# Kernel optimization log

Hardware: AMD Instinct MI355X
Metric: run time of the kernel (lower is better)

Reference implementation:

```python
import jax, jax.numpy as jnp
import numpy as np

N_NODES = 100000
N_EDGES = 1600000
N_GRAPHS = 256
IN_DIM = 64
HID = 128
LIN_HID = 128
OUT_H1, OUT_H2 = 128, 258
RELU_COEF = 0.05


def _lin_init(key, fan_in, fan_out, bias=True):
    k1, k2 = jax.random.split(key)
    bound = 1.0 / np.sqrt(fan_in)
    W = jax.random.uniform(k1, (fan_in, fan_out), minval=-bound, maxval=bound, dtype=jnp.float32)
    if bias:
        b = jax.random.uniform(k2, (fan_out,), minval=-bound, maxval=bound, dtype=jnp.float32)
        return W, b
    return W


def setup_inputs() -> dict:
    key = jax.random.key(0)
    ks = jax.random.split(key, 12)
    x = jax.random.normal(ks[0], (N_NODES, IN_DIM), dtype=jnp.float32)
    edge_index = jax.random.randint(ks[1], (2, N_EDGES), 0, N_NODES)
    batch = jnp.sort(jax.random.randint(ks[2], (N_NODES,), 0, N_GRAPHS))
    edge_attr = jax.random.uniform(ks[3], (N_EDGES,), dtype=jnp.float32)
    # GraphConv params: lin_rel (bias) applied to aggregated messages, lin_root (no bias)
    Wrel1, brel1 = _lin_init(ks[4], IN_DIM, HID)
    Wroot1 = _lin_init(ks[5], IN_DIM, HID, bias=False)
    Wrel2, brel2 = _lin_init(ks[6], HID, HID)
    Wroot2 = _lin_init(ks[7], HID, HID, bias=False)
    Wsig, bsig = _lin_init(ks[8], HID + IN_DIM, LIN_HID)
    Wtanh, btanh = _lin_init(ks[9], HID + IN_DIM, LIN_HID)
    Wf1, bf1 = _lin_init(ks[10], LIN_HID, OUT_H1)
    k11, k12 = jax.random.split(ks[11])
    Wf2, bf2 = _lin_init(k11, OUT_H1, OUT_H2)
    Wout, bout = _lin_init(k12, OUT_H2, 1)
    return dict(x=x, edge_index=edge_index, batch=batch, edge_attr=edge_attr,
                Wrel1=Wrel1, brel1=brel1, Wroot1=Wroot1,
                Wrel2=Wrel2, brel2=brel2, Wroot2=Wroot2,
                Wsig=Wsig, bsig=bsig, Wtanh=Wtanh, btanh=btanh,
                Wf1=Wf1, bf1=bf1, Wf2=Wf2, bf2=bf2, Wout=Wout, bout=bout)


def _leaky(v):
    return jnp.where(v > 0, v, RELU_COEF * v)


def _graph_conv(x, src, dst, w, Wrel, brel, Wroot):
    # out_i = Wrel @ sum_{j->i} w_ji * x_j + brel + Wroot @ x_i  (PyG GraphConv, aggr='add')
    msg = x[src] * w[:, None]                                   # [E, d]
    agg = jax.ops.segment_sum(msg, dst, num_segments=N_NODES)   # [N, d]
    return agg @ Wrel + brel + x @ Wroot


def reference(x, edge_index, batch, edge_attr,
              Wrel1, brel1, Wroot1, Wrel2, brel2, Wroot2,
              Wsig, bsig, Wtanh, btanh, Wf1, bf1, Wf2, bf2, Wout, bout):
    src, dst = edge_index[0], edge_index[1]
    x0 = x
    h = _leaky(_graph_conv(x0, src, dst, edge_attr, Wrel1, brel1, Wroot1))
    h = _leaky(_graph_conv(h, src, dst, edge_attr, Wrel2, brel2, Wroot2))
    h = jnp.concatenate([h, x0], axis=1)                        # [N, HID+IN_DIM]
    sx = jnp.clip(h @ Wsig + bsig, -30.0, 30.0)
    g = jax.nn.sigmoid(-sx) * jnp.tanh(h @ Wtanh + btanh)       # 1/(1+exp(sx)) == sigmoid(-sx)
    pooled = jax.ops.segment_sum(g, batch, num_segments=N_GRAPHS)  # [G, LIN_HID]
    f = _leaky(pooled @ Wf1 + bf1)
    f = _leaky(f @ Wf2 + bf2)
    out = jax.nn.sigmoid(f @ Wout + bout)                       # [G, 1]
    return out
```

## Files before the change

kernel.cpp:

```cpp
#include <hip/hip_runtime.h>
#include <cstdint>

#define RELU_COEF 0.05f
#define LEAKY(v) ((v) > 0.f ? (v) : RELU_COEF * (v))

typedef __attribute__((ext_vector_type(8))) short short8;
typedef __attribute__((ext_vector_type(4))) float f32x4;

#define MFMA(acc, a, b) \
    acc = __builtin_amdgcn_mfma_f32_16x16x32_bf16(a, b, acc, 0, 0, 0)

__device__ inline ushort f2bf(float f) {
    union { float f; uint32_t u; } v; v.f = f;
    return (ushort)((v.u + 0x7FFFu + ((v.u >> 16) & 1u)) >> 16);
}
__device__ inline float bf2f(ushort h) {
    union { uint32_t u; float f; } v; v.u = ((uint32_t)h) << 16;
    return v.f;
}
__device__ inline void split8(const float* p, short8& h8, short8& l8) {
    float4 a = *(const float4*)p;
    float4 b = *(const float4*)(p + 4);
    float v[8] = {a.x, a.y, a.z, a.w, b.x, b.y, b.z, b.w};
    short8 hh, ll;
#pragma unroll
    for (int i = 0; i < 8; ++i) {
        ushort hi = f2bf(v[i]);
        hh[i] = (short)hi;
        ll[i] = (short)f2bf(v[i] - bf2f(hi));
    }
    h8 = hh; l8 = ll;
}

__global__ __launch_bounds__(256) void hist_kernel(
    const int* __restrict__ ei, int* __restrict__ deg, int E)
{
    int e = blockIdx.x * 256 + threadIdx.x;
    if (e >= E) return;
    atomicAdd(&deg[ei[(size_t)E + e]], 1);
}

__global__ __launch_bounds__(256) void scan1_kernel(
    const int* __restrict__ in, int* __restrict__ out, int* __restrict__ bsum, int N)
{
    __shared__ int ts[256];
    int tid = threadIdx.x;
    int base = blockIdx.x * 1024 + tid * 4;
    int v[4];
    int s = 0;
#pragma unroll
    for (int j = 0; j < 4; ++j) {
        int idx = base + j;
        v[j] = (idx < N) ? in[idx] : 0;
        s += v[j];
    }
    ts[tid] = s;
    __syncthreads();
    for (int off = 1; off < 256; off <<= 1) {
        int t = (tid >= off) ? ts[tid - off] : 0;
        __syncthreads();
        ts[tid] += t;
        __syncthreads();
    }
    int excl = ts[tid] - s;
    if (tid == 255) bsum[blockIdx.x] = ts[255];
    int run = excl;
#pragma unroll
    for (int j = 0; j < 4; ++j) {
        int idx = base + j;
        if (idx < N) out[idx] = run;
        run += v[j];
    }
}

__global__ __launch_bounds__(512) void scan2_kernel(int* bsum, int nb)
{
    __shared__ int ts[512];
    int tid = threadIdx.x;
    int v = (tid < nb) ? bsum[tid] : 0;
    ts[tid] = v;
    __syncthreads();
    for (int off = 1; off < 512; off <<= 1) {
        int t = (tid >= off) ? ts[tid - off] : 0;
        __syncthreads();
        ts[tid] += t;
        __syncthreads();
    }
    if (tid < nb) bsum[tid] = ts[tid] - v;
}

__global__ __launch_bounds__(256) void scan3_kernel(
    int* __restrict__ rowptr, const int* __restrict__ bsum, int N, int E)
{
    int idx = blockIdx.x * 256 + threadIdx.x;
    if (idx < N) rowptr[idx] += bsum[idx >> 10];
    if (idx == 0) rowptr[N] = E;
}

#define CHUNK 4096
__global__ __launch_bounds__(256) void partA_kernel(
    const int* __restrict__ ei, const float* __restrict__ ea,
    const int* __restrict__ rowptr, int* __restrict__ bucketCursor,
    int2* __restrict__ csw2, int E, int NB)
{
    __shared__ int cnt[256];
    __shared__ int scanx[256];
    __shared__ int runc[256];
    __shared__ int gbase[256];
    __shared__ int2 staged[CHUNK];
    __shared__ unsigned char bkt[CHUNK];

    int tid = threadIdx.x;
    long long base = (long long)blockIdx.x * CHUNK;
    int cntHere = (int)((E - base) < CHUNK ? (E - base) : CHUNK);

    cnt[tid] = 0; runc[tid] = 0;
    __syncthreads();

    for (int i = tid; i < cntHere; i += 256) {
        int d = ei[(size_t)E + base + i];
        atomicAdd(&cnt[d >> 9], 1);
    }
    __syncthreads();

    int v = cnt[tid];
    scanx[tid] = v;
    __syncthreads();
    for (int off = 1; off < 256; off <<= 1) {
        int t = (tid >= off) ? scanx[tid - off] : 0;
        __syncthreads();
        scanx[tid] += t;
        __syncthreads();
    }
    int excl = scanx[tid] - v;
    if (tid < NB && v > 0)
        gbase[tid] = rowptr[tid << 9] + atomicAdd(&bucketCursor[tid], v);
    scanx[tid] = excl;
    __syncthreads();

    for (int i = tid; i < cntHere; i += 256) {
        long long e = base + i;
        int d = ei[(size_t)E + e];
        int b = d >> 9;
        int idx = scanx[b] + atomicAdd(&runc[b], 1);
        staged[idx] = make_int2(((d & 511) << 17) | ei[e], __float_as_int(ea[e]));
        bkt[idx] = (unsigned char)b;
    }
    __syncthreads();

    for (int i = tid; i < cntHere; i += 256) {
        int b = bkt[i];
        csw2[gbase[b] + (i - scanx[b])] = staged[i];
    }
}

__global__ __launch_bounds__(256) void partB_kernel(
    const int2* __restrict__ csw2, const int* __restrict__ rowptr,
    int2* __restrict__ csw, int N, int E)
{
    __shared__ int cur[512];
    int b = blockIdx.x;
    int tid = threadIdx.x;
    int node0 = b << 9;
    int nNodes = N - node0; if (nNodes > 512) nNodes = 512;
    for (int i = tid; i < nNodes; i += 256)
        cur[i] = rowptr[node0 + i];
    __syncthreads();
    int start = rowptr[node0];
    int end = (node0 + 512 >= N) ? E : rowptr[node0 + 512];
    for (int i = start + tid; i < end; i += 256) {
        int2 p = csw2[i];
        int dstLow = (int)(((unsigned)p.x) >> 17);
        int src = p.x & 0x1FFFF;
        int pos = atomicAdd(&cur[dstLow], 1);
        csw[pos] = make_int2(src, p.y);
    }
}

__global__ __launch_bounds__(256) void xbf_kernel(
    const float* __restrict__ x, ushort* __restrict__ xbf, int total4)
{
    int i = blockIdx.x * 256 + threadIdx.x;
    if (i >= total4) return;
    float4 v = *(const float4*)(x + (size_t)i * 4);
    ushort4 h;
    h.x = f2bf(v.x); h.y = f2bf(v.y); h.z = f2bf(v.z); h.w = f2bf(v.w);
    *(ushort4*)(xbf + (size_t)i * 4) = h;
}

__global__ __launch_bounds__(256) void prep_weights_kernel(
    const float* __restrict__ Wrel1, const float* __restrict__ Wroot1,
    const float* __restrict__ Wrel2, const float* __restrict__ Wroot2,
    const float* __restrict__ Wsig, const float* __restrict__ Wtanh,
    ushort* __restrict__ W1f, ushort* __restrict__ W2f, ushort* __restrict__ Wgf)
{
    int gid = blockIdx.x * 256 + threadIdx.x;
    if (gid < 32768) {
        int e = gid & 7, nn = (gid >> 3) & 127, kc = (gid >> 10) & 3;
        int hl = (gid >> 12) & 1, kk = gid >> 13;
        int k = kk * 32 + kc * 8 + e;
        float v = (k < 64) ? Wrel1[(size_t)k * 128 + nn]
                           : Wroot1[(size_t)(k - 64) * 128 + nn];
        ushort hi = f2bf(v);
        W1f[gid] = hl ? f2bf(v - bf2f(hi)) : hi;
        return;
    }
    int g2 = gid - 32768;
    if (g2 < 65536) {
        int e = g2 & 7, nn = (g2 >> 3) & 127, kc = (g2 >> 10) & 3;
        int hl = (g2 >> 12) & 1, kk = g2 >> 13;
        int k = kk * 32 + kc * 8 + e;
        float v = (k < 128) ? Wrel2[(size_t)k * 128 + nn]
                            : Wroot2[(size_t)(k - 128) * 128 + nn];
        ushort hi = f2bf(v);
        W2f[g2] = hl ? f2bf(v - bf2f(hi)) : hi;
        return;
    }
    int g3 = g2 - 65536;
    if (g3 < 98304) {
        int e = g3 & 7, nn = (g3 >> 3) & 127, kc = (g3 >> 10) & 3;
        int p = (g3 >> 12) & 3, kk = g3 >> 14;
        int k = kk * 32 + kc * 8 + e;
        float v = (p < 2) ? Wsig[(size_t)k * 128 + nn]
                          : Wtanh[(size_t)k * 128 + nn];
        ushort hi = f2bf(v);
        Wgf[g3] = (p & 1) ? f2bf(v - bf2f(hi)) : hi;
    }
}

__global__ __launch_bounds__(256) void conv1_fused_kernel(
    const float* __restrict__ x, const ushort* __restrict__ xbf,
    const int* __restrict__ rowptr, const int2* __restrict__ csw,
    const ushort* __restrict__ W1f, const float* __restrict__ brel,
    ushort* __restrict__ h1bf, int n)
{
    __shared__ __align__(16) float agg[32 * 68];

    int tid = threadIdx.x;
    int lane = tid & 63;
    int wv = tid >> 6;
    int mr = lane & 15;
    int kc = lane >> 4;
    int i0 = blockIdx.x * 32;

    {
        int q = tid & 15;
        int g = tid >> 4;
#pragma unroll
        for (int it = 0; it < 2; ++it) {
            int rl = it * 16 + g;
            int node = i0 + rl;
            float ax = 0.f, ay = 0.f, az = 0.f, aw = 0.f;
            if (node < n) {
                int b = rowptr[node], e = rowptr[node + 1];
                for (int cb = b; cb < e; cb += 16) {
                    int cnt = e - cb; if (cnt > 16) cnt = 16;
                    int sIdx = 0; float sW = 0.f;
                    if (q < cnt) {
                        int2 p = csw[cb + q];
                        sIdx = p.x; sW = __int_as_float(p.y);
                    }
                    int j = 0;
                    for (; j + 8 <= cnt; j += 8) {
                        int si[8]; float wi[8]; ushort4 fv[8];
#pragma unroll
                        for (int u = 0; u < 8; ++u) {
                            si[u] = __shfl(sIdx, j + u, 16);
                            wi[u] = __shfl(sW, j + u, 16);
                        }
#pragma unroll
                        for (int u = 0; u < 8; ++u)
                            fv[u] = *(const ushort4*)(xbf + (size_t)si[u] * 64 + q * 4);
#pragma unroll
                        for (int u = 0; u < 8; ++u) {
                            ax += wi[u] * bf2f(fv[u].x);
                            ay += wi[u] * bf2f(fv[u].y);
                            az += wi[u] * bf2f(fv[u].z);
                            aw += wi[u] * bf2f(fv[u].w);
                        }
                    }
                    for (; j < cnt; ++j) {
                        int s0 = __shfl(sIdx, j, 16); float w0 = __shfl(sW, j, 16);
                        ushort4 f0 = *(const ushort4*)(xbf + (size_t)s0 * 64 + q * 4);
                        ax += w0 * bf2f(f0.x); ay += w0 * bf2f(f0.y);
                        az += w0 * bf2f(f0.z); aw += w0 * bf2f(f0.w);
                    }
                }
            }
            *(float4*)&agg[rl * 68 + q * 4] = make_float4(ax, ay, az, aw);
        }
    }
    __syncthreads();

    int t0 = wv * 2;
    const ushort* Wp = W1f + kc * 1024 + t0 * 128 + mr * 8;
    f32x4 acc[2][2] = {};

#pragma unroll
    for (int kk = 0; kk < 2; ++kk) {
        short8 bH0 = *(const short8*)(Wp + kk * 8192);
        short8 bH1 = *(const short8*)(Wp + kk * 8192 + 128);
        short8 bL0 = *(const short8*)(Wp + kk * 8192 + 4096);
        short8 bL1 = *(const short8*)(Wp + kk * 8192 + 4096 + 128);
#pragma unroll
        for (int sub = 0; sub < 2; ++sub) {
            short8 aH, aL;
            split8(&agg[(sub * 16 + mr) * 68 + kk * 32 + kc * 8], aH, aL);
            MFMA(acc[sub][0], aH, bH0); MFMA(acc[sub][0], aH, bL0); MFMA(acc[sub][0], aL, bH0);
            MFMA(acc[sub][1], aH, bH1); MFMA(acc[sub][1], aH, bL1); MFMA(acc[sub][1], aL, bH1);
        }
    }
#pragma unroll
    for (int kk = 2; kk < 4; ++kk) {
        short8 bH0 = *(const short8*)(Wp + kk * 8192);
        short8 bH1 = *(const short8*)(Wp + kk * 8192 + 128);
        short8 bL0 = *(const short8*)(Wp + kk * 8192 + 4096);
        short8 bL1 = *(const short8*)(Wp + kk * 8192 + 4096 + 128);
#pragma unroll
        for (int sub = 0; sub < 2; ++sub) {
            int row = i0 + sub * 16 + mr; if (row > n - 1) row = n - 1;
            short8 aH, aL;
            split8(x + (size_t)row * 64 + (kk - 2) * 32 + kc * 8, aH, aL);
            MFMA(acc[sub][0], aH, bH0); MFMA(acc[sub][0], aH, bL0); MFMA(acc[sub][0], aL, bH0);
            MFMA(acc[sub][1], aH, bH1); MFMA(acc[sub][1], aH, bL1); MFMA(acc[sub][1], aL, bH1);
        }
    }

#pragma unroll
    for (int tt = 0; tt < 2; ++tt) {
        int c = (t0 + tt) * 16 + mr;
        float bv = brel[c];
#pragma unroll
        for (int sub = 0; sub < 2; ++sub)
#pragma unroll
            for (int j = 0; j < 4; ++j) {
                int r = i0 + sub * 16 + kc * 4 + j;
                if (r < n)
                    h1bf[(size_t)r * 128 + c] = f2bf(LEAKY(acc[sub][tt][j] + bv));
            }
    }
}

__global__ __launch_bounds__(256) void conv2_gate_kernel(
    const ushort* __restrict__ h1bf, const float* __restrict__ x,
    const int* __restrict__ rowptr, const int2* __restrict__ csw,
    const ushort* __restrict__ W2f, const float* __restrict__ brel,
    const ushort* __restrict__ Wgf, const float* __restrict__ bsig,
    const float* __restrict__ btanh, const int* __restrict__ batch,
    float* __restrict__ pooled, int n)
{
    __shared__ __align__(16) float agg[32 * 132];
    __shared__ int bS[32];
    float* gs = agg;

    int tid = threadIdx.x;
    int lane = tid & 63;
    int wv = tid >> 6;
    int mr = lane & 15;
    int kc = lane >> 4;
    int i0 = blockIdx.x * 32;

    {
        int q = tid & 31;
        int g = tid >> 5;
#pragma unroll
        for (int it = 0; it < 4; ++it) {
            int rl = it * 8 + g;
            int node = i0 + rl;
            float ax = 0.f, ay = 0.f, az = 0.f, aw = 0.f;
            if (node < n) {
                int b = rowptr[node], e = rowptr[node + 1];
                for (int cb = b; cb < e; cb += 32) {
                    int cnt = e - cb; if (cnt > 32) cnt = 32;
                    int sIdx = 0; float sW = 0.f;
                    if (q < cnt) {
                        int2 p = csw[cb + q];
                        sIdx = p.x; sW = __int_as_float(p.y);
                    }
                    int j = 0;
                    for (; j + 8 <= cnt; j += 8) {
                        int si[8]; float wi[8]; ushort4 fv[8];
#pragma unroll
                        for (int u = 0; u < 8; ++u) {
                            si[u] = __shfl(sIdx, j + u, 32);
                            wi[u] = __shfl(sW, j + u, 32);
                        }
#pragma unroll
                        for (int u = 0; u < 8; ++u)
                            fv[u] = *(const ushort4*)(h1bf + (size_t)si[u] * 128 + q * 4);
#pragma unroll
                        for (int u = 0; u < 8; ++u) {
                            ax += wi[u] * bf2f(fv[u].x);
                            ay += wi[u] * bf2f(fv[u].y);
                            az += wi[u] * bf2f(fv[u].z);
                            aw += wi[u] * bf2f(fv[u].w);
                        }
                    }
                    for (; j < cnt; ++j) {
                        int s0 = __shfl(sIdx, j, 32); float w0 = __shfl(sW, j, 32);
                        ushort4 f0 = *(const ushort4*)(h1bf + (size_t)s0 * 128 + q * 4);
                        ax += w0 * bf2f(f0.x); ay += w0 * bf2f(f0.y);
                        az += w0 * bf2f(f0.z); aw += w0 * bf2f(f0.w);
                    }
                }
            }
            *(float4*)&agg[rl * 132 + q * 4] = make_float4(ax, ay, az, aw);
        }
    }
    if (tid < 32) {
        int r = i0 + tid;
        bS[tid] = (r < n) ? batch[r] : -1;
    }
    __syncthreads();

    int t0 = wv * 2;

    f32x4 acc[2][2] = {};
    {
        const ushort* Wp = W2f + kc * 1024 + t0 * 128 + mr * 8;
#pragma unroll
        for (int kk = 0; kk < 4; ++kk) {
            short8 bH0 = *(const short8*)(Wp + kk * 8192);
            short8 bH1 = *(const short8*)(Wp + kk * 8192 + 128);
            short8 bL0 = *(const short8*)(Wp + kk * 8192 + 4096);
            short8 bL1 = *(const short8*)(Wp + kk * 8192 + 4096 + 128);
#pragma unroll
            for (int sub = 0; sub < 2; ++sub) {
                short8 aH, aL;
                split8(&agg[(sub * 16 + mr) * 132 + kk * 32 + kc * 8], aH, aL);
                MFMA(acc[sub][0], aH, bH0); MFMA(acc[sub][0], aH, bL0); MFMA(acc[sub][0], aL, bH0);
                MFMA(acc[sub][1], aH, bH1); MFMA(acc[sub][1], aH, bL1); MFMA(acc[sub][1], aL, bH1);
            }
        }
#pragma unroll
        for (int kk = 4; kk < 8; ++kk) {
            short8 bH0 = *(const short8*)(Wp + kk * 8192);
            short8 bH1 = *(const short8*)(Wp + kk * 8192 + 128);
            short8 bL0 = *(const short8*)(Wp + kk * 8192 + 4096);
            short8 bL1 = *(const short8*)(Wp + kk * 8192 + 4096 + 128);
#pragma unroll
            for (int sub = 0; sub < 2; ++sub) {
                int row = i0 + sub * 16 + mr; if (row > n - 1) row = n - 1;
                short8 aH = *(const short8*)(h1bf + (size_t)row * 128 + (kk - 4) * 32 + kc * 8);
                MFMA(acc[sub][0], aH, bH0); MFMA(acc[sub][0], aH, bL0);
                MFMA(acc[sub][1], aH, bH1); MFMA(acc[sub][1], aH, bL1);
            }
        }
    }
    __syncthreads();

#pragma unroll
    for (int tt = 0; tt < 2; ++tt) {
        int c = (t0 + tt) * 16 + mr;
        float bv = brel[c];
#pragma unroll
        for (int sub = 0; sub < 2; ++sub)
#pragma unroll
            for (int j = 0; j < 4; ++j) {
                int rl = sub * 16 + kc * 4 + j;
                agg[rl * 132 + c] = LEAKY(acc[sub][tt][j] + bv);
            }
    }
    __syncthreads();

    f32x4 as[2][2] = {}, at_[2][2] = {};
    {
        const ushort* Wp = Wgf + kc * 1024 + t0 * 128 + mr * 8;
#pragma unroll
        for (int kk = 0; kk < 4; ++kk) {
            short8 sH0 = *(const short8*)(Wp + kk * 16384);
            short8 sH1 = *(const short8*)(Wp + kk * 16384 + 128);
            short8 sL0 = *(const short8*)(Wp + kk * 16384 + 4096);
            short8 sL1 = *(const short8*)(Wp + kk * 16384 + 4096 + 128);
            short8 tH0 = *(const short8*)(Wp + kk * 16384 + 8192);
            short8 tH1 = *(const short8*)(Wp + kk * 16384 + 8192 + 128);
            short8 tL0 = *(const short8*)(Wp + kk * 16384 + 12288);
            short8 tL1 = *(const short8*)(Wp + kk * 16384 + 12288 + 128);
#pragma unroll
            for (int sub = 0; sub < 2; ++sub) {
                short8 aH, aL;
                split8(&agg[(sub * 16 + mr) * 132 + kk * 32 + kc * 8], aH, aL);
                MFMA(as[sub][0], aH, sH0); MFMA(as[sub][0], aH, sL0); MFMA(as[sub][0], aL, sH0);
                MFMA(as[sub][1], aH, sH1); MFMA(as[sub][1], aH, sL1); MFMA(as[sub][1], aL, sH1);
                MFMA(at_[sub][0], aH, tH0); MFMA(at_[sub][0], aH, tL0); MFMA(at_[sub][0], aL, tH0);
                MFMA(at_[sub][1], aH, tH1); MFMA(at_[sub][1], aH, tL1); MFMA(at_[sub][1], aL, tH1);
            }
        }
#pragma unroll
        for (int kk = 4; kk < 6; ++kk) {
            short8 sH0 = *(const short8*)(Wp + kk * 16384);
            short8 sH1 = *(const short8*)(Wp + kk * 16384 + 128);
            short8 sL0 = *(const short8*)(Wp + kk * 16384 + 4096);
            short8 sL1 = *(const short8*)(Wp + kk * 16384 + 4096 + 128);
            short8 tH0 = *(const short8*)(Wp + kk * 16384 + 8192);
            short8 tH1 = *(const short8*)(Wp + kk * 16384 + 8192 + 128);
            short8 tL0 = *(const short8*)(Wp + kk * 16384 + 12288);
            short8 tL1 = *(const short8*)(Wp + kk * 16384 + 12288 + 128);
#pragma unroll
            for (int sub = 0; sub < 2; ++sub) {
                int row = i0 + sub * 16 + mr; if (row > n - 1) row = n - 1;
                short8 aH, aL;
                split8(x + (size_t)row * 64 + (kk - 4) * 32 + kc * 8, aH, aL);
                MFMA(as[sub][0], aH, sH0); MFMA(as[sub][0], aH, sL0); MFMA(as[sub][0], aL, sH0);
                MFMA(as[sub][1], aH, sH1); MFMA(as[sub][1], aH, sL1); MFMA(as[sub][1], aL, sH1);
                MFMA(at_[sub][0], aH, tH0); MFMA(at_[sub][0], aH, tL0); MFMA(at_[sub][0], aL, tH0);
                MFMA(at_[sub][1], aH, tH1); MFMA(at_[sub][1], aH, tL1); MFMA(at_[sub][1], aL, tH1);
            }
        }
    }
    __syncthreads();

#pragma unroll
    for (int tt = 0; tt < 2; ++tt) {
        int c = (t0 + tt) * 16 + mr;
        float bsv = bsig[c], btv = btanh[c];
#pragma unroll
        for (int sub = 0; sub < 2; ++sub)
#pragma unroll
            for (int j = 0; j < 4; ++j) {
                int rl = sub * 16 + kc * 4 + j;
                float s = as[sub][tt][j] + bsv;
                s = fminf(fmaxf(s, -30.f), 30.f);
                float ta = at_[sub][tt][j] + btv;
                ta = fminf(fmaxf(ta, -15.f), 15.f);
                float e2 = __expf(2.f * ta);
                float th = (e2 - 1.f) / (e2 + 1.f);
                gs[rl * 128 + c] = th / (1.f + __expf(s));
            }
    }
    __syncthreads();

    int j = tid & 127;
    int m0 = (tid >> 7) * 16;
    float acc2 = 0.f;
    int cur = -1;
    for (int m = m0; m < m0 + 16; ++m) {
        int b = bS[m];
        if (b < 0) break;
        if (b != cur) {
            if (cur >= 0) atomicAdd(&pooled[(size_t)cur * 128 + j], acc2);
            cur = b;
            acc2 = 0.f;
        }
        acc2 += gs[m * 128 + j];
    }
    if (cur >= 0) atomicAdd(&pooled[(size_t)cur * 128 + j], acc2);
}

__global__ __launch_bounds__(256) void mlp_kernel(
    const float* __restrict__ pooled,
    const float* __restrict__ Wf1, const float* __restrict__ bf1,
    const float* __restrict__ Wf2, const float* __restrict__ bf2,
    const float* __restrict__ Wout, const float* __restrict__ bout,
    float* __restrict__ out)
{
    __shared__ float p[128];
    __shared__ float f1[128];
    __shared__ float f2[258];
    __shared__ float red[4];

    int g = blockIdx.x;
    int tid = threadIdx.x;

    if (tid < 128) p[tid] = pooled[(size_t)g * 128 + tid];
    __syncthreads();

    if (tid < 128) {
        float a = bf1[tid];
        for (int k = 0; k < 128; ++k) a += p[k] * Wf1[k * 128 + tid];
        f1[tid] = LEAKY(a);
    }
    __syncthreads();

    for (int j = tid; j < 258; j += 256) {
        float a = bf2[j];
        for (int k = 0; k < 128; ++k) a += f1[k] * Wf2[k * 258 + j];
        f2[j] = LEAKY(a);
    }
    __syncthreads();

    float a = 0.f;
    for (int j = tid; j < 258; j += 256) a += f2[j] * Wout[j];
#pragma unroll
    for (int off = 32; off > 0; off >>= 1) a += __shfl_down(a, off, 64);
    if ((tid & 63) == 0) red[tid >> 6] = a;
    __syncthreads();
    if (tid == 0) {
        float v = red[0] + red[1] + red[2] + red[3] + bout[0];
        out[g] = 1.f / (1.f + expf(-v));
    }
}

extern "C" void kernel_launch(void* const* d_in, const int* in_sizes, int n_in,
                              void* d_out, int out_size, void* d_ws, size_t ws_size,
                              hipStream_t stream)
{
    const float* x     = (const float*)d_in[0];
    const int*   ei    = (const int*)d_in[1];
    const int*   batch = (const int*)d_in[2];
    const float* ea    = (const float*)d_in[3];
    const float* Wrel1 = (const float*)d_in[4];
    const float* brel1 = (const float*)d_in[5];
    const float* Wroot1= (const float*)d_in[6];
    const float* Wrel2 = (const float*)d_in[7];
    const float* brel2 = (const float*)d_in[8];
    const float* Wroot2= (const float*)d_in[9];
    const float* Wsig  = (const float*)d_in[10];
    const float* bsig  = (const float*)d_in[11];
    const float* Wtanh = (const float*)d_in[12];
    const float* btanh = (const float*)d_in[13];
    const float* Wf1   = (const float*)d_in[14];
    const float* bf1   = (const float*)d_in[15];
    const float* Wf2   = (const float*)d_in[16];
    const float* bf2   = (const float*)d_in[17];
    const float* Wout  = (const float*)d_in[18];
    const float* bout  = (const float*)d_in[19];

    int N = in_sizes[2];
    int E = in_sizes[3];
    int NB = (N + 511) / 512;

    char* base = (char*)d_ws;
    size_t off = 0;
    auto alloc = [&](size_t bytes) {
        char* p = base + off;
        off += (bytes + 255) & ~(size_t)255;
        return p;
    };
    ushort*   h1bf  = (ushort*)alloc((size_t)N * 128 * 2);
    ushort*   xbf   = (ushort*)alloc((size_t)N * 64 * 2);
    int*      rowptr= (int*)alloc((size_t)(N + 1) * 4);
    int*      cursor= (int*)alloc((size_t)N * 4);
    int*      bsum  = (int*)alloc(512 * 4);
    int*      bcur  = (int*)alloc(256 * 4);
    int2*     csw   = (int2*)alloc((size_t)E * 8);
    int2*     csw2  = (int2*)alloc((size_t)E * 8);
    ushort*   W1f   = (ushort*)alloc(32768 * 2);
    ushort*   W2f   = (ushort*)alloc(65536 * 2);
    ushort*   Wgf   = (ushort*)alloc(98304 * 2);
    float*    pooled= (float*)alloc(256 * 128 * 4);

    int eblk = (E + 255) / 256;
    int nblk1 = (N + 1023) / 1024;
    int cblk = (N + 31) / 32;
    int ablk = (E + CHUNK - 1) / CHUNK;

    hipMemsetAsync(cursor, 0, (size_t)N * sizeof(int), stream);
    hipMemsetAsync(bcur, 0, 256 * sizeof(int), stream);
    hipMemsetAsync(pooled, 0, (size_t)256 * 128 * sizeof(float), stream);

    prep_weights_kernel<<<768, 256, 0, stream>>>(Wrel1, Wroot1, Wrel2, Wroot2,
                                                 Wsig, Wtanh, W1f, W2f, Wgf);
    xbf_kernel<<<(N * 16 + 255) / 256, 256, 0, stream>>>(x, xbf, N * 16);

    hist_kernel<<<eblk, 256, 0, stream>>>(ei, cursor, E);
    scan1_kernel<<<nblk1, 256, 0, stream>>>(cursor, rowptr, bsum, N);
    scan2_kernel<<<1, 512, 0, stream>>>(bsum, nblk1);
    scan3_kernel<<<(N + 255) / 256, 256, 0, stream>>>(rowptr, bsum, N, E);
    partA_kernel<<<ablk, 256, 0, stream>>>(ei, ea, rowptr, bcur, csw2, E, NB);
    partB_kernel<<<NB, 256, 0, stream>>>(csw2, rowptr, csw, N, E);

    conv1_fused_kernel<<<cblk, 256, 0, stream>>>(x, xbf, rowptr, csw,
                                                 W1f, brel1, h1bf, N);

    conv2_gate_kernel<<<cblk, 256, 0, stream>>>(h1bf, x, rowptr, csw,
                                                W2f, brel2, Wgf, bsig, btanh,
                                                batch, pooled, N);

    mlp_kernel<<<256, 256, 0, stream>>>(pooled, Wf1, bf1, Wf2, bf2, Wout, bout,
                                        (float*)d_out);
}
```

Measured before the change: 355.9 us.

## Build CSR via bucket histogram and per-bucket local scan; prefetch edge chunks

Replaces the per-node global atomic degree histogram and three-kernel scan with a shared-memory per-bucket histogram, a single 256-entry scan, and a per-bucket local histogram and scan inside partB that also writes rowptr. This removes 1.6M global atomics, an N-sized memset, and several launches. Separately, the conv gather loops now prefetch the next chunk of CSR edge entries while processing the current one, to hide load latency. The cost is an extra pass over csw2 in partB.

```diff
diff --git a/kernel.cpp b/kernel.cpp
--- a/kernel.cpp
+++ b/kernel.cpp
@@ -32,29 +32,30 @@
     h8 = hh; l8 = ll;
 }
 
-__global__ __launch_bounds__(256) void hist_kernel(
-    const int* __restrict__ ei, int* __restrict__ deg, int E)
-{
-    int e = blockIdx.x * 256 + threadIdx.x;
-    if (e >= E) return;
-    atomicAdd(&deg[ei[(size_t)E + e]], 1);
-}
-
-__global__ __launch_bounds__(256) void scan1_kernel(
-    const int* __restrict__ in, int* __restrict__ out, int* __restrict__ bsum, int N)
+#define CHUNK 4096
+
+__global__ __launch_bounds__(256) void bhist_kernel(
+    const int* __restrict__ ei, int* __restrict__ bhist, int E)
+{
+    __shared__ int cnt[256];
+    int tid = threadIdx.x;
+    cnt[tid] = 0;
+    __syncthreads();
+    long long base = (long long)blockIdx.x * CHUNK;
+    int cntHere = (int)((E - base) < CHUNK ? (E - base) : CHUNK);
+    for (int i = tid; i < cntHere; i += 256)
+        atomicAdd(&cnt[ei[(size_t)E + base + i] >> 9], 1);
+    __syncthreads();
+    if (cnt[tid] > 0) atomicAdd(&bhist[tid], cnt[tid]);
+}
+
+__global__ __launch_bounds__(256) void bscan_kernel(
+    const int* __restrict__ bhist, int* __restrict__ bptr, int E)
 {
     __shared__ int ts[256];
     int tid = threadIdx.x;
-    int base = blockIdx.x * 1024 + tid * 4;
-    int v[4];
-    int s = 0;
-#pragma unroll
-    for (int j = 0; j < 4; ++j) {
-        int idx = base + j;
-        v[j] = (idx < N) ? in[idx] : 0;
-        s += v[j];
-    }
-    ts[tid] = s;
+    int v = bhist[tid];
+    ts[tid] = v;
     __syncthreads();
     for (int off = 1; off < 256; off <<= 1) {
         int t = (tid >= off) ? ts[tid - off] : 0;
@@ -62,45 +63,13 @@
         ts[tid] += t;
         __syncthreads();
     }
-    int excl = ts[tid] - s;
-    if (tid == 255) bsum[blockIdx.x] = ts[255];
-    int run = excl;
-#pragma unroll
-    for (int j = 0; j < 4; ++j) {
-        int idx = base + j;
-        if (idx < N) out[idx] = run;
-        run += v[j];
-    }
-}
-
-__global__ __launch_bounds__(512) void scan2_kernel(int* bsum, int nb)
-{
-    __shared__ int ts[512];
-    int tid = threadIdx.x;
-    int v = (tid < nb) ? bsum[tid] : 0;
-    ts[tid] = v;
-    __syncthreads();
-    for (int off = 1; off < 512; off <<= 1) {
-        int t = (tid >= off) ? ts[tid - off] : 0;
-        __syncthreads();
-        ts[tid] += t;
-        __syncthreads();
-    }
-    if (tid < nb) bsum[tid] = ts[tid] - v;
-}
-
-__global__ __launch_bounds__(256) void scan3_kernel(
-    int* __restrict__ rowptr, const int* __restrict__ bsum, int N, int E)
-{
-    int idx = blockIdx.x * 256 + threadIdx.x;
-    if (idx < N) rowptr[idx] += bsum[idx >> 10];
-    if (idx == 0) rowptr[N] = E;
-}
-
-#define CHUNK 4096
+    bptr[tid] = ts[tid] - v;
+    if (tid == 255) bptr[256] = E;
+}
+
 __global__ __launch_bounds__(256) void partA_kernel(
     const int* __restrict__ ei, const float* __restrict__ ea,
-    const int* __restrict__ rowptr, int* __restrict__ bucketCursor,
+    const int* __restrict__ bptr, int* __restrict__ bucketCursor,
     int2* __restrict__ csw2, int E, int NB)
 {
     __shared__ int cnt[256];
@@ -134,7 +103,7 @@
     }
     int excl = scanx[tid] - v;
     if (tid < NB && v > 0)
-        gbase[tid] = rowptr[tid << 9] + atomicAdd(&bucketCursor[tid], v);
+        gbase[tid] = bptr[tid] + atomicAdd(&bucketCursor[tid], v);
     scanx[tid] = excl;
     __syncthreads();
 
@@ -155,19 +124,47 @@
 }
 
 __global__ __launch_bounds__(256) void partB_kernel(
-    const int2* __restrict__ csw2, const int* __restrict__ rowptr,
-    int2* __restrict__ csw, int N, int E)
-{
+    const int2* __restrict__ csw2, const int* __restrict__ bptr,
+    int* __restrict__ rowptr, int2* __restrict__ csw, int N, int E)
+{
+    __shared__ int hist[512];
     __shared__ int cur[512];
+    __shared__ int ts[256];
+
     int b = blockIdx.x;
     int tid = threadIdx.x;
     int node0 = b << 9;
+    int start = bptr[b], end = bptr[b + 1];
+
+    hist[tid] = 0; hist[tid + 256] = 0;
+    __syncthreads();
+    for (int i = start + tid; i < end; i += 256) {
+        int2 p = csw2[i];
+        atomicAdd(&hist[((unsigned)p.x) >> 17], 1);
+    }
+    __syncthreads();
+
+    int v0 = hist[2 * tid], v1 = hist[2 * tid + 1];
+    int s = v0 + v1;
+    ts[tid] = s;
+    __syncthreads();
+    for (int off = 1; off < 256; off <<= 1) {
+        int t = (tid >= off) ? ts[tid - off] : 0;
+        __syncthreads();
+        ts[tid] += t;
+        __syncthreads();
+    }
+    int excl = ts[tid] - s;
+    cur[2 * tid]     = start + excl;
+    cur[2 * tid + 1] = start + excl + v0;
+    __syncthreads();
+
     int nNodes = N - node0; if (nNodes > 512) nNodes = 512;
     for (int i = tid; i < nNodes; i += 256)
-        cur[i] = rowptr[node0 + i];
-    __syncthreads();
-    int start = rowptr[node0];
-    int end = (node0 + 512 >= N) ? E : rowptr[node0 + 512];
+        rowptr[node0 + i] = cur[i];
+    if (b == (int)gridDim.x - 1 && tid == 0) rowptr[N] = E;
+    __syncthreads();
+
     for (int i = start + tid; i < end; i += 256) {
         int2 p = csw2[i];
         int dstLow = (int)(((unsigned)p.x) >> 17);
@@ -253,13 +250,16 @@
             float ax = 0.f, ay = 0.f, az = 0.f, aw = 0.f;
             if (node < n) {
                 int b = rowptr[node], e = rowptr[node + 1];
-                for (int cb = b; cb < e; cb += 16) {
-                    int cnt = e - cb; if (cnt > 16) cnt = 16;
-                    int sIdx = 0; float sW = 0.f;
-                    if (q < cnt) {
-                        int2 p = csw[cb + q];
-                        sIdx = p.x; sW = __int_as_float(p.y);
-                    }
+                int cb = b;
+                int cnt = e - cb; if (cnt > 16) cnt = 16;
+                int2 pc = make_int2(0, 0);
+                if (cnt > 0 && q < cnt) pc = csw[cb + q];
+                while (cb < e) {
+                    int nb2 = cb + 16;
+                    int ncnt = e - nb2; if (ncnt > 16) ncnt = 16;
+                    int2 np = make_int2(0, 0);
+                    if (ncnt > 0 && q < ncnt) np = csw[nb2 + q];
+                    int sIdx = pc.x; float sW = __int_as_float(pc.y);
                     int j = 0;
                     for (; j + 8 <= cnt; j += 8) {
                         int si[8]; float wi[8]; ushort4 fv[8];
@@ -285,6 +285,7 @@
                         ax += w0 * bf2f(f0.x); ay += w0 * bf2f(f0.y);
                         az += w0 * bf2f(f0.z); aw += w0 * bf2f(f0.w);
                     }
+                    cb = nb2; cnt = ncnt; pc = np;
                 }
             }
             *(float4*)&agg[rl * 68 + q * 4] = make_float4(ax, ay, az, aw);
@@ -370,13 +371,16 @@
             float ax = 0.f, ay = 0.f, az = 0.f, aw = 0.f;
             if (node < n) {
                 int b = rowptr[node], e = rowptr[node + 1];
-                for (int cb = b; cb < e; cb += 32) {
-                    int cnt = e - cb; if (cnt > 32) cnt = 32;
-                    int sIdx = 0; float sW = 0.f;
-                    if (q < cnt) {
-                        int2 p = csw[cb + q];
-                        sIdx = p.x; sW = __int_as_float(p.y);
-                    }
+                int cb = b;
+                int cnt = e - cb; if (cnt > 32) cnt = 32;
+                int2 pc = make_int2(0, 0);
+                if (cnt > 0 && q < cnt) pc = csw[cb + q];
+                while (cb < e) {
+                    int nb2 = cb + 32;
+                    int ncnt = e - nb2; if (ncnt > 32) ncnt = 32;
+                    int2 np = make_int2(0, 0);
+                    if (ncnt > 0 && q < ncnt) np = csw[nb2 + q];
+                    int sIdx = pc.x; float sW = __int_as_float(pc.y);
                     int j = 0;
                     for (; j + 8 <= cnt; j += 8) {
                         int si[8]; float wi[8]; ushort4 fv[8];
@@ -402,6 +406,7 @@
                         ax += w0 * bf2f(f0.x); ay += w0 * bf2f(f0.y);
                         az += w0 * bf2f(f0.z); aw += w0 * bf2f(f0.w);
                     }
+                    cb = nb2; cnt = ncnt; pc = np;
                 }
             }
             *(float4*)&agg[rl * 132 + q * 4] = make_float4(ax, ay, az, aw);
@@ -630,8 +635,8 @@
     ushort*   h1bf  = (ushort*)alloc((size_t)N * 128 * 2);
     ushort*   xbf   = (ushort*)alloc((size_t)N * 64 * 2);
     int*      rowptr= (int*)alloc((size_t)(N + 1) * 4);
-    int*      cursor= (int*)alloc((size_t)N * 4);
-    int*      bsum  = (int*)alloc(512 * 4);
+    int*      bhist = (int*)alloc(256 * 4);
+    int*      bptr  = (int*)alloc(257 * 4);
     int*      bcur  = (int*)alloc(256 * 4);
     int2*     csw   = (int2*)alloc((size_t)E * 8);
     int2*     csw2  = (int2*)alloc((size_t)E * 8);
@@ -640,12 +645,10 @@
     ushort*   Wgf   = (ushort*)alloc(98304 * 2);
     float*    pooled= (float*)alloc(256 * 128 * 4);
 
-    int eblk = (E + 255) / 256;
-    int nblk1 = (N + 1023) / 1024;
     int cblk = (N + 31) / 32;
     int ablk = (E + CHUNK - 1) / CHUNK;
 
-    hipMemsetAsync(cursor, 0, (size_t)N * sizeof(int), stream);
+    hipMemsetAsync(bhist, 0, 256 * sizeof(int), stream);
     hipMemsetAsync(bcur, 0, 256 * sizeof(int), stream);
     hipMemsetAsync(pooled, 0, (size_t)256 * 128 * sizeof(float), stream);
 
@@ -653,12 +656,10 @@
                                                  Wsig, Wtanh, W1f, W2f, Wgf);
     xbf_kernel<<<(N * 16 + 255) / 256, 256, 0, stream>>>(x, xbf, N * 16);
 
-    hist_kernel<<<eblk, 256, 0, stream>>>(ei, cursor, E);
-    scan1_kernel<<<nblk1, 256, 0, stream>>>(cursor, rowptr, bsum, N);
-    scan2_kernel<<<1, 512, 0, stream>>>(bsum, nblk1);
-    scan3_kernel<<<(N + 255) / 256, 256, 0, stream>>>(rowptr, bsum, N, E);
-    partA_kernel<<<ablk, 256, 0, stream>>>(ei, ea, rowptr, bcur, csw2, E, NB);
-    partB_kernel<<<NB, 256, 0, stream>>>(csw2, rowptr, csw, N, E);
+    bhist_kernel<<<ablk, 256, 0, stream>>>(ei, bhist, E);
+    bscan_kernel<<<1, 256, 0, stream>>>(bhist, bptr, E);
+    partA_kernel<<<ablk, 256, 0, stream>>>(ei, ea, bptr, bcur, csw2, E, NB);
+    partB_kernel<<<NB, 256, 0, stream>>>(csw2, bptr, rowptr, csw, N, E);
 
     conv1_fused_kernel<<<cblk, 256, 0, stream>>>(x, xbf, rowptr, csw,
                                                  W1f, brel1, h1bf, N);
```

Result: faster. 303.1 us (median of 2 runs) (-14.8%).
